# Optimization experiments

Hardware: AMD Instinct MI355X
Metric: run time of the kernel (lower is better)

The kernel has to match this reference:

```python
import jax, jax.numpy as jnp
import numpy as np

B, N, D = 4, 4096, 2048
E = D // 2  # inter_channels of the non-local block


def setup_inputs() -> dict:
    key = jax.random.key(0)
    ks = jax.random.split(key, 9)
    s_in = 1.0 / np.sqrt(D)   # conv1d(k=1) default init scale, fan_in=D
    s_e = 1.0 / np.sqrt(E)    # W conv: fan_in=E
    return {
        "images_feat": jax.random.normal(ks[0], (B, N, D), jnp.float32),
        "theta_w": jax.random.uniform(ks[1], (E, D), jnp.float32, -s_in, s_in),
        "theta_b": jax.random.uniform(ks[2], (E,), jnp.float32, -s_in, s_in),
        "phi_w": jax.random.uniform(ks[3], (E, D), jnp.float32, -s_in, s_in),
        "phi_b": jax.random.uniform(ks[4], (E,), jnp.float32, -s_in, s_in),
        "g_w": jax.random.uniform(ks[5], (E, D), jnp.float32, -s_in, s_in),
        "g_b": jax.random.uniform(ks[6], (E,), jnp.float32, -s_in, s_in),
        "W_w": jax.random.uniform(ks[7], (D, E), jnp.float32, -s_e, s_e),
        "W_b": jax.random.uniform(ks[8], (D,), jnp.float32, -s_e, s_e),
    }


def reference(images_feat, theta_w, theta_b, phi_w, phi_b, g_w, g_b, W_w, W_b):
    # Original: permute (B,N,D)->(B,D,N), apply 1x1 Conv1d projections (== linear
    # over the channel dim D), theta@phi^T -> softmax -> @g, W conv back, residual,
    # permute back. Expressed directly on (B,N,D).
    x = images_feat
    theta_x = jnp.einsum("bnd,ed->bne", x, theta_w) + theta_b  # (B,N,E)
    phi_x = jnp.einsum("bnd,ed->bne", x, phi_w) + phi_b        # (B,N,E)
    g_x = jnp.einsum("bnd,ed->bne", x, g_w) + g_b              # (B,N,E)
    f = jnp.einsum("bne,bme->bnm", theta_x, phi_x)             # (B,N,N)
    attn = jax.nn.softmax(f, axis=-1)
    y = jnp.einsum("bnm,bme->bne", attn, g_x)                  # (B,N,E)
    z = jnp.einsum("bne,de->bnd", y, W_w) + W_b + x            # residual, (B,N,D)
    return z
```

## Files before the change

### kernel.cpp

```cpp
#include <hip/hip_runtime.h>

typedef short bf16x8 __attribute__((ext_vector_type(8)));
typedef _Float16 f16x8 __attribute__((ext_vector_type(8)));
typedef float f32x4 __attribute__((ext_vector_type(4)));

__device__ __forceinline__ short f2h(float f) {
  _Float16 h = (_Float16)f;
  return __builtin_bit_cast(short, h);
}
__device__ __forceinline__ float h2f(short s) {
  return (float)__builtin_bit_cast(_Float16, s);
}

__device__ __forceinline__ void gload16(const void* g, void* lds) {
  __builtin_amdgcn_global_load_lds(
      (const __attribute__((address_space(1))) unsigned*)g,
      (__attribute__((address_space(3))) unsigned*)lds, 16, 0, 0);
}

template <int NF, int K, int OMODE, int BIAS_MODE, int RES>
__global__ __launch_bounds__(512, 2) void gemm256(
    const short* __restrict__ A, int lda, long sA,
    const short* __restrict__ B, int ldb, long sB,
    void* __restrict__ Cv, int ldc, long sC,
    const float* __restrict__ bias, const float* __restrict__ resid, long sR) {
  constexpr int BN = NF * 64;
  constexpr int BNB = BN * 128;
  constexpr int NT = K / 64;
  __shared__ char lds[65536 + 2 * BNB];

  A += (size_t)blockIdx.z * sA;
  B += (size_t)blockIdx.z * sB;
  char* Cb = (char*)Cv + (size_t)blockIdx.z * sC * (OMODE == 0 ? 4 : 2);
  const float* res = resid ? resid + (size_t)blockIdx.z * sR : nullptr;

  const int tid = threadIdx.x;
  const int wid = tid >> 6, lane = tid & 63;
  const int wr = wid >> 2, wc = wid & 3;
  const int fr = lane & 15, fq = lane >> 4;
  const size_t bm = (size_t)blockIdx.y * 256;
  const size_t bn = (size_t)blockIdx.x * BN;

  const int srow = wid * 8 + (lane >> 3);
  const int scolS = ((lane & 7) * 16) ^ ((srow & 7) << 4);
  const char* Ag = (const char*)A;
  const char* Bg = (const char*)B;

  const int swz = (fr & 7) << 4;
  int aoff[8], boff[NF];
#pragma unroll
  for (int m = 0; m < 8; m++)
    aoff[m] = (wr * 128 + m * 16 + fr) * 128 + ((fq * 16) ^ swz);
#pragma unroll
  for (int n = 0; n < NF; n++)
    boff[n] = (wc * NF * 16 + n * 16 + fr) * 128 + ((fq * 16) ^ swz);

  f32x4 acc[8][NF];
#pragma unroll
  for (int m = 0; m < 8; m++)
#pragma unroll
    for (int n = 0; n < NF; n++) acc[m][n] = (f32x4){0.f, 0.f, 0.f, 0.f};

  auto stage = [&](int t, int d) {
    const int ktb = t * 128;
#pragma unroll
    for (int c = 0; c < 4; ++c)
      gload16(Ag + ((size_t)(bm + c * 64 + srow) * lda) * 2 + ktb + scolS,
              &lds[d * 32768 + c * 8192 + wid * 1024]);
#pragma unroll
    for (int c = 0; c < NF; ++c)
      gload16(Bg + ((size_t)(bn + c * 64 + srow) * ldb) * 2 + ktb + scolS,
              &lds[65536 + d * BNB + c * 8192 + wid * 1024]);
  };

  stage(0, 0);
  int cur = 0;
#pragma unroll 2
  for (int t = 0; t < NT; ++t) {
    if (t + 1 < NT) stage(t + 1, cur ^ 1);
    __builtin_amdgcn_sched_barrier(0);
    if (t + 1 < NT) {
      if constexpr (NF == 4)
        asm volatile("s_waitcnt vmcnt(8)");
      else
        asm volatile("s_waitcnt vmcnt(6)");
    } else {
      asm volatile("s_waitcnt vmcnt(0)");
    }
    __builtin_amdgcn_sched_barrier(0);
    __builtin_amdgcn_s_barrier();
    __builtin_amdgcn_sched_barrier(0);
    {
      const int dA = cur * 32768, dB = 65536 + cur * BNB;
#pragma unroll
      for (int ks = 0; ks < 2; ++ks) {
        f16x8 ar[8], br[NF];
#pragma unroll
        for (int m = 0; m < 8; m++)
          ar[m] = *(const f16x8*)&lds[dA + (aoff[m] ^ (ks << 6))];
#pragma unroll
        for (int n = 0; n < NF; n++)
          br[n] = *(const f16x8*)&lds[dB + (boff[n] ^ (ks << 6))];
#pragma unroll
        for (int m = 0; m < 8; m++)
#pragma unroll
          for (int n = 0; n < NF; n++)
            acc[m][n] = __builtin_amdgcn_mfma_f32_16x16x32_f16(
                ar[m], br[n], acc[m][n], 0, 0, 0);
      }
    }
    __builtin_amdgcn_sched_barrier(0);
    __builtin_amdgcn_s_barrier();
    __builtin_amdgcn_sched_barrier(0);
    cur ^= 1;
  }

#pragma unroll
  for (int m = 0; m < 8; m++) {
    const size_t row0 = bm + wr * 128 + m * 16 + fq * 4;
#pragma unroll
    for (int n = 0; n < NF; n++) {
      const size_t col = bn + wc * NF * 16 + n * 16 + fr;
      float bcol = (BIAS_MODE == 1) ? bias[col] : 0.f;
#pragma unroll
      for (int r = 0; r < 4; r++) {
        float val = acc[m][n][r];
        const size_t row = row0 + r;
        const size_t idx = row * (size_t)ldc + col;
        if (BIAS_MODE == 1) val += bcol;
        if (BIAS_MODE == 2) val += bias[row];
        if (RES) val += res[idx];
        if (OMODE == 0)
          ((float*)Cb)[idx] = val;
        else
          ((short*)Cb)[idx] = f2h(val);
      }
    }
  }
}

__global__ __launch_bounds__(256) void cvt_f32_f16(const float* __restrict__ s,
                                                   short* __restrict__ d, int n) {
  int i = (blockIdx.x * 256 + threadIdx.x) * 8;
  if (i >= n) return;
  const float4 a = *(const float4*)(s + i);
  const float4 b = *(const float4*)(s + i + 4);
  bf16x8 o;
  o[0] = f2h(a.x); o[1] = f2h(a.y); o[2] = f2h(a.z); o[3] = f2h(a.w);
  o[4] = f2h(b.x); o[5] = f2h(b.y); o[6] = f2h(b.z); o[7] = f2h(b.w);
  *(bf16x8*)(d + i) = o;
}

__global__ __launch_bounds__(256) void cvt_weights(
    const float* __restrict__ thw, const float* __restrict__ phw,
    const float* __restrict__ gw, const float* __restrict__ Ww,
    short* __restrict__ wcat, short* __restrict__ gwb, short* __restrict__ wWb,
    const float* __restrict__ thb, const float* __restrict__ phb,
    float* __restrict__ bc) {
  const int b = blockIdx.x;
  const int seg = b >> 10, ib = b & 1023;
  const float* s;
  short* d;
  if (seg == 0) { s = thw; d = wcat; }
  else if (seg == 1) { s = phw; d = wcat + 2097152; }
  else if (seg == 2) { s = gw; d = gwb; }
  else { s = Ww; d = wWb; }
  const int i = (ib * 256 + threadIdx.x) * 8;
  const float4 a = *(const float4*)(s + i);
  const float4 v = *(const float4*)(s + i + 4);
  bf16x8 o;
  o[0] = f2h(a.x); o[1] = f2h(a.y); o[2] = f2h(a.z); o[3] = f2h(a.w);
  o[4] = f2h(v.x); o[5] = f2h(v.y); o[6] = f2h(v.z); o[7] = f2h(v.w);
  *(bf16x8*)(d + i) = o;
  if (b == 0) {
    const int j = threadIdx.x * 8;
#pragma unroll
    for (int k = 0; k < 8; ++k) {
      const int jj = j + k;
      bc[jj] = (jj < 1024) ? thb[jj] : phb[jj - 1024];
    }
  }
}

__global__ __launch_bounds__(256) void softmax_rows(short* __restrict__ S) {
  const size_t row = blockIdx.x;
  short* rp = S + row * 4096;
  const int tid = threadIdx.x;
  const int lane = tid & 63, wid = tid >> 6;
  float v[16];
#pragma unroll
  for (int c = 0; c < 2; c++) {
    bf16x8 xv = *(const bf16x8*)(rp + (c * 256 + tid) * 8);
#pragma unroll
    for (int j = 0; j < 8; j++) v[c * 8 + j] = h2f(xv[j]);
  }
  float m = v[0];
#pragma unroll
  for (int i = 1; i < 16; i++) m = fmaxf(m, v[i]);
#pragma unroll
  for (int off = 32; off >= 1; off >>= 1) m = fmaxf(m, __shfl_xor(m, off));
  __shared__ float red[8];
  if (lane == 0) red[wid] = m;
  __syncthreads();
  m = fmaxf(fmaxf(red[0], red[1]), fmaxf(red[2], red[3]));
  float s = 0.f;
#pragma unroll
  for (int i = 0; i < 16; i++) {
    v[i] = __expf(v[i] - m);
    s += v[i];
  }
#pragma unroll
  for (int off = 32; off >= 1; off >>= 1) s += __shfl_xor(s, off);
  if (lane == 0) red[4 + wid] = s;
  __syncthreads();
  s = (red[4] + red[5]) + (red[6] + red[7]);
  const float rs = 1.0f / s;
#pragma unroll
  for (int c = 0; c < 2; c++) {
    bf16x8 o;
#pragma unroll
    for (int j = 0; j < 8; j++) o[j] = f2h(v[c * 8 + j] * rs);
    *(bf16x8*)(rp + (c * 256 + tid) * 8) = o;
  }
}

extern "C" void kernel_launch(void* const* d_in, const int* in_sizes, int n_in,
                              void* d_out, int out_size, void* d_ws,
                              size_t ws_size, hipStream_t stream) {
  const float* x   = (const float*)d_in[0];
  const float* thw = (const float*)d_in[1];
  const float* thb = (const float*)d_in[2];
  const float* phw = (const float*)d_in[3];
  const float* phb = (const float*)d_in[4];
  const float* gw  = (const float*)d_in[5];
  const float* gbi = (const float*)d_in[6];
  const float* Ww  = (const float*)d_in[7];
  const float* Wb  = (const float*)d_in[8];
  float* out = (float*)d_out;

  char* ws = (char*)d_ws;
  short* xf   = (short*)(ws);
  short* wcat = (short*)(ws + 67108864);
  short* gwb  = (short*)(ws + 75497472);
  short* wWb  = (short*)(ws + 79691776);
  float* bc   = (float*)(ws + 83886080);
  short* tpf  = (short*)(ws + 83894272);
  short* gT   = (short*)(ws + 151003136);
  short* sc   = (short*)(ws);

  cvt_f32_f16<<<16384, 256, 0, stream>>>(x, xf, 33554432);
  cvt_weights<<<4096, 256, 0, stream>>>(thw, phw, gw, Ww, wcat, gwb, wWb, thb,
                                        phb, bc);

  gemm256<4, 2048, 1, 1, 0><<<dim3(8, 64, 1), 512, 0, stream>>>(
      xf, 2048, 0L, wcat, 2048, 0L, tpf, 2048, 0L, bc, nullptr, 0L);

  gemm256<4, 2048, 1, 2, 0><<<dim3(16, 4, 4), 512, 0, stream>>>(
      gwb, 2048, 0L, xf, 2048, 8388608L, gT, 4096, 4194304L, gbi, nullptr, 0L);

  for (int p = 0; p < 2; ++p) {
    const short* tp = tpf + (size_t)p * 16777216;
    gemm256<4, 1024, 1, 0, 0><<<dim3(16, 16, 2), 512, 0, stream>>>(
        tp, 2048, 8388608L, tp + 1024, 2048, 8388608L,
        sc, 4096, 16777216L, nullptr, nullptr, 0L);
    softmax_rows<<<8192, 256, 0, stream>>>(sc);
    short* yp = tpf + (size_t)p * 16777216;
    gemm256<2, 4096, 1, 0, 0><<<dim3(8, 16, 2), 512, 0, stream>>>(
        sc, 4096, 16777216L, gT + (size_t)p * 8388608, 4096, 4194304L,
        yp, 1024, 4194304L, nullptr, nullptr, 0L);
    gemm256<4, 1024, 0, 1, 1><<<dim3(8, 16, 2), 512, 0, stream>>>(
        yp, 1024, 4194304L, wWb, 1024, 0L,
        out + (size_t)p * 16777216, 2048, 8388608L,
        Wb, x + (size_t)p * 16777216, 8388608L);
  }
}
```

Measured before the change: 703.5 us.

## Interleave LDS fragment loads with MFMA phases using barriers and setprio

Splits the inner GEMM tile into phases, each loading a few A/B fragments from LDS and then issuing MFMAs, separated by workgroup barriers with lgkmcnt waits. s_setprio raises wave priority during MFMA bursts so waves desynchronise and overlap LDS reads with matrix math. It also drops the unroll-by-2 of the k loop and cuts live fragment registers. The added barriers per k-step may add sync overhead, and the accumulation order changes slightly.

```diff
diff --git a/kernel.cpp b/kernel.cpp
--- a/kernel.cpp
+++ b/kernel.cpp
@@ -19,7 +19,7 @@
 }
 
 template <int NF, int K, int OMODE, int BIAS_MODE, int RES>
-__global__ __launch_bounds__(512, 2) void gemm256(
+__global__ __launch_bounds__(512, 2) void gemmph(
     const short* __restrict__ A, int lda, long sA,
     const short* __restrict__ B, int ldb, long sB,
     void* __restrict__ Cv, int ldc, long sC,
@@ -73,11 +73,16 @@
               &lds[65536 + d * BNB + c * 8192 + wid * 1024]);
   };
 
+#define SBAR                             \
+  __builtin_amdgcn_sched_barrier(0);     \
+  __builtin_amdgcn_s_barrier();          \
+  __builtin_amdgcn_sched_barrier(0);     \
+  asm volatile("s_waitcnt lgkmcnt(0)");  \
+  __builtin_amdgcn_sched_barrier(0)
+
   stage(0, 0);
-  int cur = 0;
-#pragma unroll 2
   for (int t = 0; t < NT; ++t) {
-    if (t + 1 < NT) stage(t + 1, cur ^ 1);
+    if (t + 1 < NT) stage(t + 1, (t + 1) & 1);
     __builtin_amdgcn_sched_barrier(0);
     if (t + 1 < NT) {
       if constexpr (NF == 4)
@@ -90,30 +95,101 @@
     __builtin_amdgcn_sched_barrier(0);
     __builtin_amdgcn_s_barrier();
     __builtin_amdgcn_sched_barrier(0);
-    {
-      const int dA = cur * 32768, dB = 65536 + cur * BNB;
-#pragma unroll
-      for (int ks = 0; ks < 2; ++ks) {
-        f16x8 ar[8], br[NF];
-#pragma unroll
-        for (int m = 0; m < 8; m++)
-          ar[m] = *(const f16x8*)&lds[dA + (aoff[m] ^ (ks << 6))];
-#pragma unroll
-        for (int n = 0; n < NF; n++)
-          br[n] = *(const f16x8*)&lds[dB + (boff[n] ^ (ks << 6))];
-#pragma unroll
-        for (int m = 0; m < 8; m++)
-#pragma unroll
-          for (int n = 0; n < NF; n++)
-            acc[m][n] = __builtin_amdgcn_mfma_f32_16x16x32_f16(
-                ar[m], br[n], acc[m][n], 0, 0, 0);
-      }
-    }
+
+    const int dA = (t & 1) * 32768, dB = 65536 + (t & 1) * BNB;
+    f16x8 aA[4], aB[4], b0[NF], b1[NF];
+
+    aA[0] = *(const f16x8*)&lds[dA + aoff[0]];
+    aA[1] = *(const f16x8*)&lds[dA + (aoff[0] ^ 64)];
+    aA[2] = *(const f16x8*)&lds[dA + aoff[1]];
+    aA[3] = *(const f16x8*)&lds[dA + (aoff[1] ^ 64)];
+#pragma unroll
+    for (int n = 0; n < NF; n++) b0[n] = *(const f16x8*)&lds[dB + boff[n]];
+    SBAR;
+    __builtin_amdgcn_s_setprio(1);
+#pragma unroll
+    for (int n = 0; n < NF; n++) {
+      acc[0][n] = __builtin_amdgcn_mfma_f32_16x16x32_f16(aA[0], b0[n],
+                                                         acc[0][n], 0, 0, 0);
+      acc[1][n] = __builtin_amdgcn_mfma_f32_16x16x32_f16(aA[2], b0[n],
+                                                         acc[1][n], 0, 0, 0);
+    }
+    __builtin_amdgcn_s_setprio(0);
+
+#pragma unroll
+    for (int n = 0; n < NF; n++)
+      b1[n] = *(const f16x8*)&lds[dB + (boff[n] ^ 64)];
+    aB[0] = *(const f16x8*)&lds[dA + aoff[2]];
+    aB[1] = *(const f16x8*)&lds[dA + (aoff[2] ^ 64)];
+    aB[2] = *(const f16x8*)&lds[dA + aoff[3]];
+    aB[3] = *(const f16x8*)&lds[dA + (aoff[3] ^ 64)];
+    SBAR;
+    __builtin_amdgcn_s_setprio(1);
+#pragma unroll
+    for (int n = 0; n < NF; n++) {
+      acc[0][n] = __builtin_amdgcn_mfma_f32_16x16x32_f16(aA[1], b1[n],
+                                                         acc[0][n], 0, 0, 0);
+      acc[1][n] = __builtin_amdgcn_mfma_f32_16x16x32_f16(aA[3], b1[n],
+                                                         acc[1][n], 0, 0, 0);
+    }
+    __builtin_amdgcn_s_setprio(0);
+
+    aA[0] = *(const f16x8*)&lds[dA + aoff[4]];
+    aA[1] = *(const f16x8*)&lds[dA + (aoff[4] ^ 64)];
+    aA[2] = *(const f16x8*)&lds[dA + aoff[5]];
+    aA[3] = *(const f16x8*)&lds[dA + (aoff[5] ^ 64)];
+    SBAR;
+    __builtin_amdgcn_s_setprio(1);
+#pragma unroll
+    for (int n = 0; n < NF; n++) {
+      acc[2][n] = __builtin_amdgcn_mfma_f32_16x16x32_f16(aB[0], b0[n],
+                                                         acc[2][n], 0, 0, 0);
+      acc[2][n] = __builtin_amdgcn_mfma_f32_16x16x32_f16(aB[1], b1[n],
+                                                         acc[2][n], 0, 0, 0);
+      acc[3][n] = __builtin_amdgcn_mfma_f32_16x16x32_f16(aB[2], b0[n],
+                                                         acc[3][n], 0, 0, 0);
+      acc[3][n] = __builtin_amdgcn_mfma_f32_16x16x32_f16(aB[3], b1[n],
+                                                         acc[3][n], 0, 0, 0);
+    }
+    __builtin_amdgcn_s_setprio(0);
+
+    aB[0] = *(const f16x8*)&lds[dA + aoff[6]];
+    aB[1] = *(const f16x8*)&lds[dA + (aoff[6] ^ 64)];
+    aB[2] = *(const f16x8*)&lds[dA + aoff[7]];
+    aB[3] = *(const f16x8*)&lds[dA + (aoff[7] ^ 64)];
+    SBAR;
+    __builtin_amdgcn_s_setprio(1);
+#pragma unroll
+    for (int n = 0; n < NF; n++) {
+      acc[4][n] = __builtin_amdgcn_mfma_f32_16x16x32_f16(aA[0], b0[n],
+                                                         acc[4][n], 0, 0, 0);
+      acc[4][n] = __builtin_amdgcn_mfma_f32_16x16x32_f16(aA[1], b1[n],
+                                                         acc[4][n], 0, 0, 0);
+      acc[5][n] = __builtin_amdgcn_mfma_f32_16x16x32_f16(aA[2], b0[n],
+                                                         acc[5][n], 0, 0, 0);
+      acc[5][n] = __builtin_amdgcn_mfma_f32_16x16x32_f16(aA[3], b1[n],
+                                                         acc[5][n], 0, 0, 0);
+    }
+    __builtin_amdgcn_s_setprio(0);
+
+    __builtin_amdgcn_s_setprio(1);
+#pragma unroll
+    for (int n = 0; n < NF; n++) {
+      acc[6][n] = __builtin_amdgcn_mfma_f32_16x16x32_f16(aB[0], b0[n],
+                                                         acc[6][n], 0, 0, 0);
+      acc[6][n] = __builtin_amdgcn_mfma_f32_16x16x32_f16(aB[1], b1[n],
+                                                         acc[6][n], 0, 0, 0);
+      acc[7][n] = __builtin_amdgcn_mfma_f32_16x16x32_f16(aB[2], b0[n],
+                                                         acc[7][n], 0, 0, 0);
+      acc[7][n] = __builtin_amdgcn_mfma_f32_16x16x32_f16(aB[3], b1[n],
+                                                         acc[7][n], 0, 0, 0);
+    }
+    __builtin_amdgcn_s_setprio(0);
     __builtin_amdgcn_sched_barrier(0);
     __builtin_amdgcn_s_barrier();
     __builtin_amdgcn_sched_barrier(0);
-    cur ^= 1;
-  }
+  }
+#undef SBAR
 
 #pragma unroll
   for (int m = 0; m < 8; m++) {
@@ -252,23 +328,23 @@
   cvt_weights<<<4096, 256, 0, stream>>>(thw, phw, gw, Ww, wcat, gwb, wWb, thb,
                                         phb, bc);
 
-  gemm256<4, 2048, 1, 1, 0><<<dim3(8, 64, 1), 512, 0, stream>>>(
+  gemmph<4, 2048, 1, 1, 0><<<dim3(8, 64, 1), 512, 0, stream>>>(
       xf, 2048, 0L, wcat, 2048, 0L, tpf, 2048, 0L, bc, nullptr, 0L);
 
-  gemm256<4, 2048, 1, 2, 0><<<dim3(16, 4, 4), 512, 0, stream>>>(
+  gemmph<4, 2048, 1, 2, 0><<<dim3(16, 4, 4), 512, 0, stream>>>(
       gwb, 2048, 0L, xf, 2048, 8388608L, gT, 4096, 4194304L, gbi, nullptr, 0L);
 
   for (int p = 0; p < 2; ++p) {
     const short* tp = tpf + (size_t)p * 16777216;
-    gemm256<4, 1024, 1, 0, 0><<<dim3(16, 16, 2), 512, 0, stream>>>(
+    gemmph<4, 1024, 1, 0, 0><<<dim3(16, 16, 2), 512, 0, stream>>>(
         tp, 2048, 8388608L, tp + 1024, 2048, 8388608L,
         sc, 4096, 16777216L, nullptr, nullptr, 0L);
     softmax_rows<<<8192, 256, 0, stream>>>(sc);
     short* yp = tpf + (size_t)p * 16777216;
-    gemm256<2, 4096, 1, 0, 0><<<dim3(8, 16, 2), 512, 0, stream>>>(
+    gemmph<2, 4096, 1, 0, 0><<<dim3(8, 16, 2), 512, 0, stream>>>(
         sc, 4096, 16777216L, gT + (size_t)p * 8388608, 4096, 4194304L,
         yp, 1024, 4194304L, nullptr, nullptr, 0L);
-    gemm256<4, 1024, 0, 1, 1><<<dim3(8, 16, 2), 512, 0, stream>>>(
+    gemmph<4, 1024, 0, 1, 1><<<dim3(8, 16, 2), 512, 0, stream>>>(
         yp, 1024, 4194304L, wWb, 1024, 0L,
         out + (size_t)p * 16777216, 2048, 8388608L,
         Wb, x + (size_t)p * 16777216, 8388608L);
```

Result: no change. 700.6 us (-0.4%).
